# Optimization experiments

Hardware: AMD Instinct MI355X
Metric: run time of the kernel (lower is better)

The kernel has to match this reference:

```python
import jax, jax.numpy as jnp
import numpy as np

B, C, F_, T = 32, 2, 1024, 512
CF = C * F_
H = 128  # lstm hidden / embedding dim


def setup_inputs() -> dict:
    key = jax.random.key(0)
    ks = jax.random.split(key, 12)
    s = 0.05
    return {
        "x": jax.random.normal(ks[0], (B, C, F_, T), dtype=jnp.float32),
        "W_fc1": jax.random.normal(ks[1], (H, CF), dtype=jnp.float32) * s,
        "b_fc1": jax.random.normal(ks[2], (H,), dtype=jnp.float32) * s,
        "Wih_f": jax.random.normal(ks[3], (4 * H, H), dtype=jnp.float32) * s,
        "Whh_f": jax.random.normal(ks[4], (4 * H, H), dtype=jnp.float32) * s,
        "b_f": jax.random.normal(ks[5], (4 * H,), dtype=jnp.float32) * s,
        "Wih_b": jax.random.normal(ks[6], (4 * H, H), dtype=jnp.float32) * s,
        "Whh_b": jax.random.normal(ks[7], (4 * H, H), dtype=jnp.float32) * s,
        "b_b": jax.random.normal(ks[8], (4 * H,), dtype=jnp.float32) * s,
        "W_out": jax.random.normal(ks[9], (H, 2 * H), dtype=jnp.float32) * s,
        "b_out": jax.random.normal(ks[10], (H,), dtype=jnp.float32) * s,
    }


def _lstm_scan(x, Wih, Whh, b):
    # x: (L, T, H); recurrence over L (torch treats the (B,128) input as an
    # unbatched sequence of length B), vectorized over the T frames.
    L, Tn, _ = x.shape
    Hn = Whh.shape[1]

    def step(carry, xt):
        h, c = carry  # (T, H)
        z = xt @ Wih.T + h @ Whh.T + b  # (T, 4H)
        i, f, g, o = jnp.split(z, 4, axis=-1)
        c = jax.nn.sigmoid(f) * c + jax.nn.sigmoid(i) * jnp.tanh(g)
        h = jax.nn.sigmoid(o) * jnp.tanh(c)
        return (h, c), h

    init = (jnp.zeros((Tn, Hn), x.dtype), jnp.zeros((Tn, Hn), x.dtype))
    _, hs = jax.lax.scan(step, init, x)
    return hs  # (L, T, H)


def reference(x, W_fc1, b_fc1, Wih_f, Whh_f, b_f, Wih_b, Whh_b, b_b, W_out, b_out):
    Bn, Cn, Fn, Tn = x.shape
    # fc1 applied per time frame: (B, CF, T) -> (B, T, 128)
    xr = x.reshape(Bn, Cn * Fn, Tn).transpose(0, 2, 1)
    h = jnp.einsum("btc,dc->btd", xr, W_fc1) + b_fc1
    # bidirectional LSTM over the batch axis (torch unbatched-input semantics)
    hf = _lstm_scan(h, Wih_f, Whh_f, b_f)
    hb = _lstm_scan(h[::-1], Wih_b, Whh_b, b_b)[::-1]
    hs = jnp.concatenate([hf, hb], axis=-1)  # (B, T, 256)
    out = jnp.einsum("btd,ed->bte", hs, W_out) + b_out  # (B, T, 128)
    return out.transpose(0, 2, 1)  # (B, 128, T), matching torch.stack(dim=2)
```

## Files before the change

kernel.cpp:

```cpp
#include <hip/hip_runtime.h>
#include <stdint.h>

typedef __attribute__((ext_vector_type(8))) short short8;
typedef __attribute__((ext_vector_type(4))) float floatx4;

__device__ __forceinline__ float bf16_to_f(uint16_t u) {
    union { uint32_t i; float f; } v; v.i = ((uint32_t)u) << 16; return v.f;
}
__device__ __forceinline__ uint16_t f_to_bf16(float f) {
    union { uint32_t i; float f; } v; v.f = f;
    uint32_t u = v.i;
    u += 0x7FFFu + ((u >> 16) & 1u);
    return (uint16_t)(u >> 16);
}
__device__ __forceinline__ void gload16(const void* g, void* l) {
    __builtin_amdgcn_global_load_lds(
        (const __attribute__((address_space(1))) void*)g,
        (__attribute__((address_space(3))) void*)l, 16, 0, 0);
}
__device__ __forceinline__ float rcpf(float x) { return __builtin_amdgcn_rcpf(x); }

__device__ __forceinline__ void bar_lds() {
    asm volatile("s_waitcnt lgkmcnt(0)" ::: "memory");
    __builtin_amdgcn_s_barrier();
    asm volatile("" ::: "memory");
}

#define B_  32
#define T_  512
#define CF_ 2048
#define H_  128
#define G4_ 512
#define BT_ 16384
#define LOG2E 1.4426950408889634f

__global__ __launch_bounds__(256) void k_cvt_all(
        const float* __restrict__ Wfc, const float* __restrict__ Wih_f,
        const float* __restrict__ Wih_b, const float* __restrict__ Whh_f,
        const float* __restrict__ Whh_b, const float* __restrict__ Wout,
        uint16_t* __restrict__ WfcB, uint16_t* __restrict__ WihB,
        uint16_t* __restrict__ WhhB, uint16_t* __restrict__ WoutB) {
    const int blk = blockIdx.x;
    const float* s; uint16_t* d; int off;
    if (blk < 256)      { s = Wfc;   d = WfcB;          off = blk; }
    else if (blk < 320) { s = Wih_f; d = WihB;          off = blk - 256; }
    else if (blk < 384) { s = Wih_b; d = WihB + 65536;  off = blk - 320; }
    else if (blk < 448) { s = Whh_f; d = WhhB;          off = blk - 384; }
    else if (blk < 512) { s = Whh_b; d = WhhB + 65536;  off = blk - 448; }
    else                { s = Wout;  d = WoutB;         off = blk - 512; }
    const int i = off * 1024 + threadIdx.x * 4;
    float4 v = *(const float4*)&s[i];
    ushort4 o;
    o.x = f_to_bf16(v.x); o.y = f_to_bf16(v.y);
    o.z = f_to_bf16(v.z); o.w = f_to_bf16(v.w);
    *(ushort4*)&d[i] = o;
}

__global__ __launch_bounds__(512) void k_fc1a(const float* __restrict__ x,
                                              const uint16_t* __restrict__ WfcB,
                                              float* __restrict__ Hpart) {
    __shared__ float tile[64 * 65];
    __shared__ __align__(16) uint16_t As[8192];
    __shared__ __align__(16) uint16_t Bs[4224];

    const int bb = blockIdx.y, n0 = blockIdx.x * 64, kc = blockIdx.z;
    const int kbase = kc * 512;
    const int tid = threadIdx.x, w = tid >> 6, l = tid & 63;
    const int lm = l & 15, lk = l >> 4;
    const float* xb = x + (size_t)bb * CF_ * T_;

    const int t4 = (tid & 15) * 4, cf_r = tid >> 4;
    const int kk = (tid & 15) * 4, t_r = tid >> 4;

    float4 xv0, xv1;
    {
        const float* p = &xb[(size_t)(kbase + cf_r) * T_ + n0 + t4];
        xv0 = *(const float4*)p;
        xv1 = *(const float4*)(p + 32 * T_);
    }

    const int wmA = (w >> 1) * 32, wnA = (w & 1) * 32;
    floatx4 acc[2][2] = {};
    for (int i = 0; i < 8; ++i) {
        const int k0 = kbase + i * 64;
        __syncthreads();
        tile[(t4 + 0) * 65 + cf_r] = xv0.x;
        tile[(t4 + 1) * 65 + cf_r] = xv0.y;
        tile[(t4 + 2) * 65 + cf_r] = xv0.z;
        tile[(t4 + 3) * 65 + cf_r] = xv0.w;
        tile[(t4 + 0) * 65 + cf_r + 32] = xv1.x;
        tile[(t4 + 1) * 65 + cf_r + 32] = xv1.y;
        tile[(t4 + 2) * 65 + cf_r + 32] = xv1.z;
        tile[(t4 + 3) * 65 + cf_r + 32] = xv1.w;
        gload16(WfcB + (size_t)l * CF_ + k0 + w * 8,        As + (w * 128 + l) * 8);
        gload16(WfcB + (size_t)(64 + l) * CF_ + k0 + w * 8, As + (w * 128 + 64 + l) * 8);
        __syncthreads();
        if (i < 7) {
            const float* p = &xb[(size_t)(k0 + 64 + cf_r) * T_ + n0 + t4];
            xv0 = *(const float4*)p;
            xv1 = *(const float4*)(p + 32 * T_);
        }
        #pragma unroll
        for (int pass = 0; pass < 2; ++pass) {
            const int tr = t_r + pass * 32;
            ushort4 o;
            o.x = f_to_bf16(tile[tr * 65 + kk + 0]);
            o.y = f_to_bf16(tile[tr * 65 + kk + 1]);
            o.z = f_to_bf16(tile[tr * 65 + kk + 2]);
            o.w = f_to_bf16(tile[tr * 65 + kk + 3]);
            *(ushort4*)&Bs[((kk >> 3) * 66 + tr) * 8 + (kk & 7)] = o;
        }
        __syncthreads();
        short8 a[2][2], bfr[2][2];
        #pragma unroll
        for (int kf = 0; kf < 2; ++kf) {
            #pragma unroll
            for (int mf = 0; mf < 2; ++mf)
                a[mf][kf] = *(const short8*)&As[((kf * 4 + lk) * 128 + wmA + mf * 16 + lm) * 8];
            #pragma unroll
            for (int nf = 0; nf < 2; ++nf)
                bfr[nf][kf] = *(const short8*)&Bs[((kf * 4 + lk) * 66 + wnA + nf * 16 + lm) * 8];
        }
        #pragma unroll
        for (int mf = 0; mf < 2; ++mf)
            #pragma unroll
            for (int nf = 0; nf < 2; ++nf) {
                acc[mf][nf] = __builtin_amdgcn_mfma_f32_16x16x32_bf16(a[mf][0], bfr[nf][0], acc[mf][nf], 0, 0, 0);
                acc[mf][nf] = __builtin_amdgcn_mfma_f32_16x16x32_bf16(a[mf][1], bfr[nf][1], acc[mf][nf], 0, 0, 0);
            }
    }
    float* Hp = Hpart + (size_t)kc * H_ * BT_;
    #pragma unroll
    for (int mf = 0; mf < 2; ++mf) {
        const int d0 = wmA + mf * 16 + lk * 4;
        #pragma unroll
        for (int nf = 0; nf < 2; ++nf) {
            const int bt = bb * T_ + n0 + wnA + nf * 16 + lm;
            #pragma unroll
            for (int r = 0; r < 4; ++r)
                Hp[(size_t)(d0 + r) * BT_ + bt] = acc[mf][nf][r];
        }
    }
}

__global__ __launch_bounds__(256) void k_hsum(const float* __restrict__ Hpart,
                                              const float* __restrict__ bfc,
                                              uint16_t* __restrict__ Hcm) {
    const int d = blockIdx.y, bt = blockIdx.x * 1024 + threadIdx.x * 4;
    const float b = bfc[d];
    float4 s = *(const float4*)&Hpart[(size_t)d * BT_ + bt];
    #pragma unroll
    for (int kc = 1; kc < 4; ++kc) {
        const float4 v = *(const float4*)&Hpart[(size_t)kc * H_ * BT_ + (size_t)d * BT_ + bt];
        s.x += v.x; s.y += v.y; s.z += v.z; s.w += v.w;
    }
    uint16_t* o = Hcm + ((size_t)(d >> 3) * BT_ + bt) * 8 + (d & 7);
    o[0]  = f_to_bf16(s.x + b);
    o[8]  = f_to_bf16(s.y + b);
    o[16] = f_to_bf16(s.z + b);
    o[24] = f_to_bf16(s.w + b);
}

__global__ __launch_bounds__(256) void k_xproj(const uint16_t* __restrict__ Hcm,
                                               const uint16_t* __restrict__ WihB,
                                               const float* __restrict__ b_f,
                                               const float* __restrict__ b_b,
                                               uint16_t* __restrict__ Xp) {
    __shared__ __align__(16) uint16_t As[64 * 136];
    __shared__ __align__(16) uint16_t Bs[16 * 66 * 8];
    const int bt0 = blockIdx.x * 64, gy = blockIdx.y;
    const int dir = gy >> 3;
    const int gl0 = gy * 64 - dir * 512;
    const int tid = threadIdx.x, w = tid >> 6, l = tid & 63;
    const int lm = l & 15, lk = l >> 4;

    #pragma unroll
    for (int j = 0; j < 4; ++j) {
        const int c = w * 4 + j;
        gload16(Hcm + ((size_t)c * BT_ + bt0 + l) * 8, Bs + (c * 66 + l) * 8);
    }
    {
        const int r = tid >> 2, c4 = tid & 3;
        const uint16_t* src = WihB + (size_t)(gy * 64 + r) * H_ + c4 * 32;
        short8 v0 = *(const short8*)(src);
        short8 v1 = *(const short8*)(src + 8);
        short8 v2 = *(const short8*)(src + 16);
        short8 v3 = *(const short8*)(src + 24);
        uint16_t* dst = &As[r * 136 + c4 * 32];
        *(short8*)(dst)      = v0;
        *(short8*)(dst + 8)  = v1;
        *(short8*)(dst + 16) = v2;
        *(short8*)(dst + 24) = v3;
    }
    __syncthreads();

    const int wm = (w >> 1) * 32, wn = (w & 1) * 32;
    short8 a[2][4], bfr[2][4];
    #pragma unroll
    for (int kf = 0; kf < 4; ++kf) {
        #pragma unroll
        for (int mf = 0; mf < 2; ++mf)
            a[mf][kf] = *(const short8*)&As[(wm + mf * 16 + lm) * 136 + kf * 32 + lk * 8];
        #pragma unroll
        for (int nf = 0; nf < 2; ++nf)
            bfr[nf][kf] = *(const short8*)&Bs[((kf * 4 + lk) * 66 + wn + nf * 16 + lm) * 8];
    }
    floatx4 acc[2][2] = {};
    #pragma unroll
    for (int kf = 0; kf < 4; ++kf)
        #pragma unroll
        for (int mf = 0; mf < 2; ++mf)
            #pragma unroll
            for (int nf = 0; nf < 2; ++nf)
                acc[mf][nf] = __builtin_amdgcn_mfma_f32_16x16x32_bf16(a[mf][kf], bfr[nf][kf], acc[mf][nf], 0, 0, 0);

    const float* bi = dir ? b_b : b_f;
    #pragma unroll
    for (int mf = 0; mf < 2; ++mf) {
        const int g = gl0 + wm + mf * 16 + lk * 4;
        const float4 bv = *(const float4*)&bi[g];
        #pragma unroll
        for (int nf = 0; nf < 2; ++nf) {
            const int bt = bt0 + wn + nf * 16 + lm;
            const int bb = bt >> 9, t = bt & 511;
            ushort4 o;
            o.x = f_to_bf16(acc[mf][nf][0] + bv.x);
            o.y = f_to_bf16(acc[mf][nf][1] + bv.y);
            o.z = f_to_bf16(acc[mf][nf][2] + bv.z);
            o.w = f_to_bf16(acc[mf][nf][3] + bv.w);
            *(ushort4*)&Xp[((size_t)(dir * B_ + bb) * T_ + t) * G4_ + g] = o;
        }
    }
}

__global__ __launch_bounds__(512) void k_lstm(const uint16_t* __restrict__ Xp,
                                              const uint16_t* __restrict__ WhhB,
                                              uint16_t* __restrict__ hs) {
    __shared__ __align__(16) uint16_t h_sh[2][16 * 136];
    const int dir = blockIdx.y, t0 = blockIdx.x * 16;
    const int tid = threadIdx.x, w = tid >> 6, l = tid & 63;
    const int lm = l & 15, lk = l >> 4;
    const int gcol = w * 16 + lm;
    const int tloc = lk * 4;
    const uint16_t* Wp = WhhB + dir * (G4_ * H_);

    short8 bw[4][4];
    #pragma unroll
    for (int q = 0; q < 4; ++q)
        #pragma unroll
        for (int kf = 0; kf < 4; ++kf)
            bw[q][kf] = *(const short8*)&Wp[(size_t)(q * H_ + gcol) * H_ + kf * 32 + lk * 8];

    for (int i = tid; i < 16 * 136; i += 512) h_sh[0][i] = 0;
    float c[4] = {0.f, 0.f, 0.f, 0.f};

    uint16_t xva[4][4], xvb[4][4];
    {
        const int b0 = dir ? (B_ - 1) : 0;
        const uint16_t* xp = Xp + ((size_t)(dir * B_ + b0) * T_ + t0 + tloc) * G4_;
        #pragma unroll
        for (int r = 0; r < 4; ++r)
            #pragma unroll
            for (int q = 0; q < 4; ++q)
                xva[r][q] = xp[(size_t)r * G4_ + q * H_ + gcol];
    }
    bar_lds();

    auto step = [&](int s, uint16_t (&xc)[4][4], uint16_t (&xn)[4][4], int par) {
        const int b_idx = dir ? (B_ - 1 - s) : s;
        short8 af[4];
        #pragma unroll
        for (int kf = 0; kf < 4; ++kf)
            af[kf] = *(const short8*)&h_sh[par][lm * 136 + kf * 32 + lk * 8];
        floatx4 acc[4] = {};
        #pragma unroll
        for (int q = 0; q < 4; ++q)
            #pragma unroll
            for (int kf = 0; kf < 4; ++kf)
                acc[q] = __builtin_amdgcn_mfma_f32_16x16x32_bf16(af[kf], bw[q][kf], acc[q], 0, 0, 0);
        if (s < B_ - 1) {
            const int bn = dir ? (B_ - 2 - s) : (s + 1);
            const uint16_t* xp = Xp + ((size_t)(dir * B_ + bn) * T_ + t0 + tloc) * G4_;
            #pragma unroll
            for (int r = 0; r < 4; ++r)
                #pragma unroll
                for (int q = 0; q < 4; ++q)
                    xn[r][q] = xp[(size_t)r * G4_ + q * H_ + gcol];
        }
        #pragma unroll
        for (int r = 0; r < 4; ++r) {
            float zi = acc[0][r] + bf16_to_f(xc[r][0]);
            float zf = acc[1][r] + bf16_to_f(xc[r][1]);
            float zg = acc[2][r] + bf16_to_f(xc[r][2]);
            float zo = acc[3][r] + bf16_to_f(xc[r][3]);
            float si = rcpf(1.f + __builtin_amdgcn_exp2f(-LOG2E * zi));
            float sf = rcpf(1.f + __builtin_amdgcn_exp2f(-LOG2E * zf));
            float so = rcpf(1.f + __builtin_amdgcn_exp2f(-LOG2E * zo));
            float tg = 1.f - 2.f * rcpf(1.f + __builtin_amdgcn_exp2f(2.f * LOG2E * zg));
            c[r] = sf * c[r] + si * tg;
            float tc = 1.f - 2.f * rcpf(1.f + __builtin_amdgcn_exp2f(2.f * LOG2E * c[r]));
            float hn = so * tc;
            uint16_t hb = f_to_bf16(hn);
            h_sh[par ^ 1][(tloc + r) * 136 + gcol] = hb;
            hs[((size_t)b_idx * T_ + t0 + tloc + r) * 256 + dir * H_ + gcol] = hb;
        }
        bar_lds();
    };

    for (int s2 = 0; s2 < 16; ++s2) {
        step(2 * s2,     xva, xvb, 0);
        step(2 * s2 + 1, xvb, xva, 1);
    }
}

__global__ __launch_bounds__(256) void k_outm(const uint16_t* __restrict__ WoutB,
                                              const uint16_t* __restrict__ hs,
                                              const float* __restrict__ bout,
                                              float* __restrict__ out) {
    __shared__ __align__(16) uint16_t As[4096], Bs[4096];
    const int b = blockIdx.z, m0 = blockIdx.y * 64, n0 = blockIdx.x * 64;
    const int tid = threadIdx.x, w = tid >> 6, l = tid & 63;
    const int wm = (w >> 1) * 32, wn = (w & 1) * 32;
    const int lm = l & 15, lk = l >> 4;
    const uint16_t* A = WoutB + (size_t)m0 * 256;
    const uint16_t* Bp = hs + ((size_t)b * T_ + n0) * 256;
    floatx4 acc[2][2] = {};
    const uint16_t* gA = A + (size_t)l * 256;
    const uint16_t* gB = Bp + (size_t)l * 256;
    for (int k0 = 0; k0 < 256; k0 += 64) {
        __syncthreads();
        gload16(gA + k0 + (2 * w) * 8,     As + ((2 * w) * 64 + l) * 8);
        gload16(gA + k0 + (2 * w + 1) * 8, As + ((2 * w + 1) * 64 + l) * 8);
        gload16(gB + k0 + (2 * w) * 8,     Bs + ((2 * w) * 64 + l) * 8);
        gload16(gB + k0 + (2 * w + 1) * 8, Bs + ((2 * w + 1) * 64 + l) * 8);
        __syncthreads();
        short8 a[2][2], bfr[2][2];
        #pragma unroll
        for (int kf = 0; kf < 2; ++kf) {
            #pragma unroll
            for (int mf = 0; mf < 2; ++mf)
                a[mf][kf] = *(const short8*)&As[((kf * 4 + lk) * 64 + wm + mf * 16 + lm) * 8];
            #pragma unroll
            for (int nf = 0; nf < 2; ++nf)
                bfr[nf][kf] = *(const short8*)&Bs[((kf * 4 + lk) * 64 + wn + nf * 16 + lm) * 8];
        }
        #pragma unroll
        for (int mf = 0; mf < 2; ++mf)
            #pragma unroll
            for (int nf = 0; nf < 2; ++nf) {
                acc[mf][nf] = __builtin_amdgcn_mfma_f32_16x16x32_bf16(a[mf][0], bfr[nf][0], acc[mf][nf], 0, 0, 0);
                acc[mf][nf] = __builtin_amdgcn_mfma_f32_16x16x32_bf16(a[mf][1], bfr[nf][1], acc[mf][nf], 0, 0, 0);
            }
    }
    #pragma unroll
    for (int mf = 0; mf < 2; ++mf) {
        const int e0 = m0 + wm + mf * 16 + lk * 4;
        const float4 bv = *(const float4*)&bout[e0];
        #pragma unroll
        for (int nf = 0; nf < 2; ++nf) {
            const int t = n0 + wn + nf * 16 + lm;
            out[((size_t)b * H_ + e0 + 0) * T_ + t] = acc[mf][nf][0] + bv.x;
            out[((size_t)b * H_ + e0 + 1) * T_ + t] = acc[mf][nf][1] + bv.y;
            out[((size_t)b * H_ + e0 + 2) * T_ + t] = acc[mf][nf][2] + bv.z;
            out[((size_t)b * H_ + e0 + 3) * T_ + t] = acc[mf][nf][3] + bv.w;
        }
    }
}

extern "C" void kernel_launch(void* const* d_in, const int* in_sizes, int n_in,
                              void* d_out, int out_size, void* d_ws, size_t ws_size,
                              hipStream_t stream) {
    const float* x     = (const float*)d_in[0];
    const float* Wfc   = (const float*)d_in[1];
    const float* bfc   = (const float*)d_in[2];
    const float* Wih_f = (const float*)d_in[3];
    const float* Whh_f = (const float*)d_in[4];
    const float* b_f   = (const float*)d_in[5];
    const float* Wih_b = (const float*)d_in[6];
    const float* Whh_b = (const float*)d_in[7];
    const float* b_b   = (const float*)d_in[8];
    const float* Wout  = (const float*)d_in[9];
    const float* bout  = (const float*)d_in[10];
    float* out = (float*)d_out;

    char* ws = (char*)d_ws;
    uint16_t* Xp    = (uint16_t*)(ws);
    uint16_t* hsB   = (uint16_t*)(ws + 33554432);
    float*    Hpart = (float*)   (ws + 41943040);
    uint16_t* Hcm   = (uint16_t*)(ws + 75497472);
    uint16_t* WfcB  = (uint16_t*)(ws + 79691776);
    uint16_t* WihB  = (uint16_t*)(ws + 80216064);
    uint16_t* WhhB  = (uint16_t*)(ws + 80478208);
    uint16_t* WoutB = (uint16_t*)(ws + 80740352);

    k_cvt_all<<<dim3(544), 256, 0, stream>>>(Wfc, Wih_f, Wih_b, Whh_f, Whh_b, Wout,
                                             WfcB, WihB, WhhB, WoutB);
    k_fc1a <<<dim3(8, 32, 4), 512, 0, stream>>>(x, WfcB, Hpart);
    k_hsum <<<dim3(16, 128),  256, 0, stream>>>(Hpart, bfc, Hcm);
    k_xproj<<<dim3(256, 16),  256, 0, stream>>>(Hcm, WihB, b_f, b_b, Xp);
    k_lstm <<<dim3(32, 2),    512, 0, stream>>>(Xp, WhhB, hsB);
    k_outm <<<dim3(8, 2, 32), 256, 0, stream>>>(WoutB, hsB, bout, out);
}
```

Before: 300.8 us.

## Rewrite fc1 GEMM with pre-swizzled weights and direct global fragment loads

Converts W_fc1 to bf16 in a swizzled layout matching MFMA A-fragment order and replaces the LDS-tiled fc1 kernel with one that reads x and weight fragments directly from global memory, one wave per K quarter over 16 frames. This removes LDS transposes and block barriers in the GEMM. In exchange, x is read with strided narrow loads that may coalesce poorly, and weights are re-read from cache by every block.

```diff
diff --git a/kernel.cpp b/kernel.cpp
--- a/kernel.cpp
+++ b/kernel.cpp
@@ -38,12 +38,23 @@
         const float* __restrict__ Wfc, const float* __restrict__ Wih_f,
         const float* __restrict__ Wih_b, const float* __restrict__ Whh_f,
         const float* __restrict__ Whh_b, const float* __restrict__ Wout,
-        uint16_t* __restrict__ WfcB, uint16_t* __restrict__ WihB,
+        uint16_t* __restrict__ WswzB, uint16_t* __restrict__ WihB,
         uint16_t* __restrict__ WhhB, uint16_t* __restrict__ WoutB) {
     const int blk = blockIdx.x;
+    if (blk < 256) {
+        const int i = blk * 1024 + threadIdx.x * 4;
+        const int d = i >> 11, k = i & 2047;
+        float4 v = *(const float4*)&Wfc[i];
+        ushort4 o;
+        o.x = f_to_bf16(v.x); o.y = f_to_bf16(v.y);
+        o.z = f_to_bf16(v.z); o.w = f_to_bf16(v.w);
+        const int kc = k >> 5, lk = (k >> 3) & 3, e = k & 7;
+        const int mf = d >> 4, lm = d & 15;
+        *(ushort4*)&WswzB[(size_t)(((kc * 8 + mf) * 64 + lk * 16 + lm) * 8 + e)] = o;
+        return;
+    }
     const float* s; uint16_t* d; int off;
-    if (blk < 256)      { s = Wfc;   d = WfcB;          off = blk; }
-    else if (blk < 320) { s = Wih_f; d = WihB;          off = blk - 256; }
+    if (blk < 320)      { s = Wih_f; d = WihB;          off = blk - 256; }
     else if (blk < 384) { s = Wih_b; d = WihB + 65536;  off = blk - 320; }
     else if (blk < 448) { s = Whh_f; d = WhhB;          off = blk - 384; }
     else if (blk < 512) { s = Whh_b; d = WhhB + 65536;  off = blk - 448; }
@@ -56,90 +67,42 @@
     *(ushort4*)&d[i] = o;
 }
 
-__global__ __launch_bounds__(512) void k_fc1a(const float* __restrict__ x,
-                                              const uint16_t* __restrict__ WfcB,
+__global__ __launch_bounds__(256) void k_fc1w(const float* __restrict__ x,
+                                              const uint16_t* __restrict__ Wswz,
                                               float* __restrict__ Hpart) {
-    __shared__ float tile[64 * 65];
-    __shared__ __align__(16) uint16_t As[8192];
-    __shared__ __align__(16) uint16_t Bs[4224];
-
-    const int bb = blockIdx.y, n0 = blockIdx.x * 64, kc = blockIdx.z;
-    const int kbase = kc * 512;
     const int tid = threadIdx.x, w = tid >> 6, l = tid & 63;
     const int lm = l & 15, lk = l >> 4;
-    const float* xb = x + (size_t)bb * CF_ * T_;
-
-    const int t4 = (tid & 15) * 4, cf_r = tid >> 4;
-    const int kk = (tid & 15) * 4, t_r = tid >> 4;
-
-    float4 xv0, xv1;
-    {
-        const float* p = &xb[(size_t)(kbase + cf_r) * T_ + n0 + t4];
-        xv0 = *(const float4*)p;
-        xv1 = *(const float4*)(p + 32 * T_);
-    }
-
-    const int wmA = (w >> 1) * 32, wnA = (w & 1) * 32;
-    floatx4 acc[2][2] = {};
-    for (int i = 0; i < 8; ++i) {
-        const int k0 = kbase + i * 64;
-        __syncthreads();
-        tile[(t4 + 0) * 65 + cf_r] = xv0.x;
-        tile[(t4 + 1) * 65 + cf_r] = xv0.y;
-        tile[(t4 + 2) * 65 + cf_r] = xv0.z;
-        tile[(t4 + 3) * 65 + cf_r] = xv0.w;
-        tile[(t4 + 0) * 65 + cf_r + 32] = xv1.x;
-        tile[(t4 + 1) * 65 + cf_r + 32] = xv1.y;
-        tile[(t4 + 2) * 65 + cf_r + 32] = xv1.z;
-        tile[(t4 + 3) * 65 + cf_r + 32] = xv1.w;
-        gload16(WfcB + (size_t)l * CF_ + k0 + w * 8,        As + (w * 128 + l) * 8);
-        gload16(WfcB + (size_t)(64 + l) * CF_ + k0 + w * 8, As + (w * 128 + 64 + l) * 8);
-        __syncthreads();
-        if (i < 7) {
-            const float* p = &xb[(size_t)(k0 + 64 + cf_r) * T_ + n0 + t4];
-            xv0 = *(const float4*)p;
-            xv1 = *(const float4*)(p + 32 * T_);
-        }
-        #pragma unroll
-        for (int pass = 0; pass < 2; ++pass) {
-            const int tr = t_r + pass * 32;
-            ushort4 o;
-            o.x = f_to_bf16(tile[tr * 65 + kk + 0]);
-            o.y = f_to_bf16(tile[tr * 65 + kk + 1]);
-            o.z = f_to_bf16(tile[tr * 65 + kk + 2]);
-            o.w = f_to_bf16(tile[tr * 65 + kk + 3]);
-            *(ushort4*)&Bs[((kk >> 3) * 66 + tr) * 8 + (kk & 7)] = o;
-        }
-        __syncthreads();
-        short8 a[2][2], bfr[2][2];
-        #pragma unroll
-        for (int kf = 0; kf < 2; ++kf) {
-            #pragma unroll
-            for (int mf = 0; mf < 2; ++mf)
-                a[mf][kf] = *(const short8*)&As[((kf * 4 + lk) * 128 + wmA + mf * 16 + lm) * 8];
-            #pragma unroll
-            for (int nf = 0; nf < 2; ++nf)
-                bfr[nf][kf] = *(const short8*)&Bs[((kf * 4 + lk) * 66 + wnA + nf * 16 + lm) * 8];
-        }
-        #pragma unroll
-        for (int mf = 0; mf < 2; ++mf)
-            #pragma unroll
-            for (int nf = 0; nf < 2; ++nf) {
-                acc[mf][nf] = __builtin_amdgcn_mfma_f32_16x16x32_bf16(a[mf][0], bfr[nf][0], acc[mf][nf], 0, 0, 0);
-                acc[mf][nf] = __builtin_amdgcn_mfma_f32_16x16x32_bf16(a[mf][1], bfr[nf][1], acc[mf][nf], 0, 0, 0);
-            }
-    }
-    float* Hp = Hpart + (size_t)kc * H_ * BT_;
-    #pragma unroll
-    for (int mf = 0; mf < 2; ++mf) {
-        const int d0 = wmA + mf * 16 + lk * 4;
-        #pragma unroll
-        for (int nf = 0; nf < 2; ++nf) {
-            const int bt = bb * T_ + n0 + wnA + nf * 16 + lm;
-            #pragma unroll
-            for (int r = 0; r < 4; ++r)
-                Hp[(size_t)(d0 + r) * BT_ + bt] = acc[mf][nf][r];
-        }
+    const int bt0 = blockIdx.x * 16;
+    const int bb = bt0 >> 9, t0 = bt0 & 511;
+    const int kc4 = w;
+    const float* xb = x + ((size_t)bb * CF_ + kc4 * 512) * T_ + t0 + lm;
+
+    floatx4 acc[8] = {};
+    #pragma unroll 2
+    for (int s = 0; s < 16; ++s) {
+        const int kk = s * 32;
+        float xv[8];
+        #pragma unroll
+        for (int j = 0; j < 8; ++j)
+            xv[j] = xb[(size_t)(kk + lk * 8 + j) * T_];
+        short8 bfr;
+        #pragma unroll
+        for (int j = 0; j < 8; ++j)
+            bfr[j] = (short)f_to_bf16(xv[j]);
+        const uint16_t* wp = Wswz + ((size_t)(kc4 * 16 + s) * 8 * 64 + l) * 8;
+        #pragma unroll
+        for (int mf = 0; mf < 8; ++mf) {
+            short8 a = *(const short8*)(wp + mf * 512);
+            acc[mf] = __builtin_amdgcn_mfma_f32_16x16x32_bf16(a, bfr, acc[mf], 0, 0, 0);
+        }
+    }
+    float* Hp = Hpart + (size_t)kc4 * H_ * BT_;
+    #pragma unroll
+    for (int mf = 0; mf < 8; ++mf) {
+        const int d0 = mf * 16 + lk * 4;
+        #pragma unroll
+        for (int r = 0; r < 4; ++r)
+            Hp[(size_t)(d0 + r) * BT_ + bt0 + lm] = acc[mf][r];
     }
 }
 
@@ -388,14 +351,14 @@
     uint16_t* hsB   = (uint16_t*)(ws + 33554432);
     float*    Hpart = (float*)   (ws + 41943040);
     uint16_t* Hcm   = (uint16_t*)(ws + 75497472);
-    uint16_t* WfcB  = (uint16_t*)(ws + 79691776);
+    uint16_t* Wswz  = (uint16_t*)(ws + 79691776);
     uint16_t* WihB  = (uint16_t*)(ws + 80216064);
     uint16_t* WhhB  = (uint16_t*)(ws + 80478208);
     uint16_t* WoutB = (uint16_t*)(ws + 80740352);
 
     k_cvt_all<<<dim3(544), 256, 0, stream>>>(Wfc, Wih_f, Wih_b, Whh_f, Whh_b, Wout,
-                                             WfcB, WihB, WhhB, WoutB);
-    k_fc1a <<<dim3(8, 32, 4), 512, 0, stream>>>(x, WfcB, Hpart);
+                                             Wswz, WihB, WhhB, WoutB);
+    k_fc1w <<<dim3(1024),     256, 0, stream>>>(x, Wswz, Hpart);
     k_hsum <<<dim3(16, 128),  256, 0, stream>>>(Hpart, bfc, Hcm);
     k_xproj<<<dim3(256, 16),  256, 0, stream>>>(Hcm, WihB, b_f, b_b, Xp);
     k_lstm <<<dim3(32, 2),    512, 0, stream>>>(Xp, WhhB, hsB);
```

Result: slower. 332.5 us (+10.5%).
